# Optimization experiments

Measured on AMD Instinct MI355X. Metric: run time of the kernel, lower is better.

Reference implementation:

```python
import jax, jax.numpy as jnp
import numpy as np

B, S, E, H = 1, 4096, 768, 12
D = E // H  # headSize = 64

def setup_inputs() -> dict:
    key = jax.random.key(0)
    ks = jax.random.split(key, 7)
    scale = 1.0 / np.sqrt(E)
    return {
        "inputQueries": jax.random.normal(ks[0], (B, S, E), dtype=jnp.float32),
        "inputKeys":    jax.random.normal(ks[1], (B, S, E), dtype=jnp.float32),
        "inputValues":  jax.random.normal(ks[2], (B, S, E), dtype=jnp.float32),
        "Wq": jax.random.normal(ks[3], (E, E), dtype=jnp.float32) * scale,
        "Wk": jax.random.normal(ks[4], (E, E), dtype=jnp.float32) * scale,
        "Wv": jax.random.normal(ks[5], (E, E), dtype=jnp.float32) * scale,
        "Wo": jax.random.normal(ks[6], (E, E), dtype=jnp.float32) * scale,
    }

def reference(inputQueries, inputKeys, inputValues, Wq, Wk, Wv, Wo):
    # nn.Linear(x) = x @ W.T; weights stored as [out, in]
    q = inputQueries @ Wq.T  # [B,S,E]
    k = inputKeys @ Wk.T
    v = inputValues @ Wv.T
    # split heads -> [B,H,S,D]
    q = q.reshape(B, S, H, D).transpose(0, 2, 1, 3)
    k = k.reshape(B, S, H, D).transpose(0, 2, 1, 3)
    v = v.reshape(B, S, H, D).transpose(0, 2, 1, 3)
    # full QK^T scores [B,H,S,S] (faithful to the naive implementation)
    scores = jnp.einsum("bhqd,bhkd->bhqk", q, k) / jnp.sqrt(jnp.float32(D))
    attn = jax.nn.softmax(scores, axis=-1)
    # (mask path in original is a discarded non-inplace masked_fill -> no-op;
    #  dropout=0.0 -> identity)
    ctx = jnp.einsum("bhqk,bhkd->bhqd", attn, v)  # [B,H,S,D]
    ctx = ctx.transpose(0, 2, 1, 3).reshape(B, S, E)
    return ctx @ Wo.T
```

## Files before the change

kernel.cpp:

```cpp
#include <hip/hip_runtime.h>

#define SS 4096
#define EE 768
#define HH 12
#define DD 64

typedef __attribute__((ext_vector_type(4))) float f32x4;
typedef __attribute__((ext_vector_type(8))) _Float16 f16x8;
typedef __attribute__((ext_vector_type(4))) _Float16 f16x4;
typedef __attribute__((ext_vector_type(8))) unsigned short u16x8;

__global__ __launch_bounds__(256) void cast_kernel(
    const float* __restrict__ xq, const float* __restrict__ xk,
    const float* __restrict__ xv, const float* __restrict__ wq,
    const float* __restrict__ wk, const float* __restrict__ wv,
    const float* __restrict__ wo, _Float16* __restrict__ oxq,
    _Float16* __restrict__ oxk, _Float16* __restrict__ oxv,
    _Float16* __restrict__ owq, _Float16* __restrict__ owk,
    _Float16* __restrict__ owv, _Float16* __restrict__ owo) {
    const int seg = blockIdx.y;
    const float* src;
    _Float16* dst;
    int n;
    float s = 1.0f;
    switch (seg) {
        case 0: src = xq; dst = oxq; n = SS * EE; break;
        case 1: src = xk; dst = oxk; n = SS * EE; break;
        case 2: src = xv; dst = oxv; n = SS * EE; break;
        case 3: src = wq; dst = owq; n = EE * EE; s = 0.125f; break;
        case 4: src = wk; dst = owk; n = EE * EE; break;
        case 5: src = wv; dst = owv; n = EE * EE; break;
        default: src = wo; dst = owo; n = EE * EE; break;
    }
    const int i = (blockIdx.x * 256 + threadIdx.x) * 4;
    if (i < n) {
        const float4 v = *(const float4*)(src + i);
        f16x4 o;
        o[0] = (_Float16)(v.x * s); o[1] = (_Float16)(v.y * s);
        o[2] = (_Float16)(v.z * s); o[3] = (_Float16)(v.w * s);
        *(f16x4*)(dst + i) = o;
    }
}

template <bool F32OUT>
__device__ __forceinline__ void gemm_f16_body(const _Float16* __restrict__ A,
                                              const _Float16* __restrict__ B,
                                              void* __restrict__ Yv) {
    __shared__ _Float16 As[128 * 32];
    __shared__ _Float16 Bs[128 * 32];

    const int tid = threadIdx.x;
    const int w = tid >> 6, lane = tid & 63;
    const int g = lane >> 4, c = lane & 15;
    const int wr = (w >> 1) * 64, wc = (w & 1) * 64;
    const int m0 = blockIdx.y * 128, n0 = blockIdx.x * 128;

    f32x4 acc[4][4] = {};

    for (int k0 = 0; k0 < EE; k0 += 32) {
        __syncthreads();
#pragma unroll
        for (int i = 0; i < 2; ++i) {
            const int ca = tid + i * 256;
            __builtin_amdgcn_global_load_lds(
                (const __attribute__((address_space(1))) void*)(
                    A + (size_t)(m0 + (ca >> 2)) * EE + k0 + (ca & 3) * 8),
                (__attribute__((address_space(3))) void*)(As + ca * 8), 16, 0, 0);
            __builtin_amdgcn_global_load_lds(
                (const __attribute__((address_space(1))) void*)(
                    B + (size_t)(n0 + (ca >> 2)) * EE + k0 + (ca & 3) * 8),
                (__attribute__((address_space(3))) void*)(Bs + ca * 8), 16, 0, 0);
        }
        __syncthreads();

        f16x8 af[4], bf[4];
#pragma unroll
        for (int t = 0; t < 4; ++t) {
            af[t] = *(const f16x8*)(As + (wr + t * 16 + c) * 32 + g * 8);
            bf[t] = *(const f16x8*)(Bs + (wc + t * 16 + c) * 32 + g * 8);
        }
#pragma unroll
        for (int mt = 0; mt < 4; ++mt)
#pragma unroll
            for (int nt = 0; nt < 4; ++nt)
                acc[mt][nt] = __builtin_amdgcn_mfma_f32_16x16x32_f16(
                    af[mt], bf[nt], acc[mt][nt], 0, 0, 0);
    }

    if (F32OUT) {
        float* Y = (float*)Yv;
#pragma unroll
        for (int mt = 0; mt < 4; ++mt)
#pragma unroll
            for (int nt = 0; nt < 4; ++nt)
#pragma unroll
                for (int r = 0; r < 4; ++r)
                    Y[(size_t)(m0 + wr + mt * 16 + g * 4 + r) * EE +
                      n0 + wc + nt * 16 + c] = acc[mt][nt][r];
    } else {
        _Float16* Y = (_Float16*)Yv;
#pragma unroll
        for (int mt = 0; mt < 4; ++mt)
#pragma unroll
            for (int nt = 0; nt < 4; ++nt)
#pragma unroll
                for (int r = 0; r < 4; ++r)
                    Y[(size_t)(m0 + wr + mt * 16 + g * 4 + r) * EE +
                      n0 + wc + nt * 16 + c] = (_Float16)acc[mt][nt][r];
    }
}

__global__ __launch_bounds__(256) void qkv_gemm_kernel(
    const _Float16* __restrict__ Xq, const _Float16* __restrict__ Xk,
    const _Float16* __restrict__ Xv, const _Float16* __restrict__ Wq,
    const _Float16* __restrict__ Wk, const _Float16* __restrict__ Wv,
    _Float16* __restrict__ Yq, _Float16* __restrict__ Yk,
    _Float16* __restrict__ Yv) {
    const int z = blockIdx.z;
    const _Float16* X = (z == 0) ? Xq : (z == 1) ? Xk : Xv;
    const _Float16* W = (z == 0) ? Wq : (z == 1) ? Wk : Wv;
    _Float16* Y = (z == 0) ? Yq : (z == 1) ? Yk : Yv;
    gemm_f16_body<false>(X, W, (void*)Y);
}

__global__ __launch_bounds__(256) void out_gemm_kernel(
    const _Float16* __restrict__ X, const _Float16* __restrict__ W,
    float* __restrict__ Y) {
    gemm_f16_body<true>(X, W, (void*)Y);
}

__global__ __launch_bounds__(128) void attn_mfma_kernel(
    const _Float16* __restrict__ Qf, const _Float16* __restrict__ Kf,
    const _Float16* __restrict__ Vf, _Float16* __restrict__ C) {
    __shared__ _Float16 Ks[2][64 * 64];
    __shared__ unsigned char VtB[2][64 * 144];

    const int tid = threadIdx.x;
    const int bid = blockIdx.x;
    const int sw = (bid & 7) * 96 + (bid >> 3);
    const int h = sw >> 6;
    const int q0 = (sw & 63) * 64;
    const int w = tid >> 6;
    const int lane = tid & 63;
    const int g = lane >> 4;
    const int c = lane & 15;

    const int vr2 = tid >> 3;
    const int vm = tid & 7;

    f16x8 qa[2][2];
#pragma unroll
    for (int qf = 0; qf < 2; ++qf) {
        const _Float16* qp =
            Qf + (size_t)(q0 + w * 32 + qf * 16 + c) * EE + h * DD + g * 8;
        qa[qf][0] = *(const f16x8*)(qp);
        qa[qf][1] = *(const f16x8*)(qp + 32);
    }

    f32x4 o[2][4] = {};
    float m_q[2] = {-1e30f, -1e30f}, l_q[2] = {0.0f, 0.0f};
    u16x8 vreg[2][2];

#define ISSUE_K(buf, t0k)                                                     \
    {                                                                          \
        _Pragma("unroll") for (int i = 0; i < 4; ++i) {                        \
            const int L = i * 128 + tid;                                       \
            const int r_ = L >> 3;                                             \
            const int cc_ = (L & 7) ^ (r_ & 7);                                \
            __builtin_amdgcn_global_load_lds(                                  \
                (const __attribute__((address_space(1))) void*)(               \
                    Kf + (size_t)((t0k) + r_) * EE + h * DD + cc_ * 8),        \
                (__attribute__((address_space(3))) void*)(&Ks[buf][L * 8]),    \
                16, 0, 0);                                                     \
        }                                                                      \
    }
#define LOAD_V(t0v)                                                           \
    {                                                                          \
        _Pragma("unroll") for (int u = 0; u < 2; ++u) {                        \
            const int vrr = vr2 + 16 * u;                                      \
            const unsigned short* vp = (const unsigned short*)(                \
                Vf + (size_t)((t0v) + 2 * vrr) * EE + h * DD + vm * 8);        \
            vreg[u][0] = *(const u16x8*)(vp);                                  \
            vreg[u][1] = *(const u16x8*)(vp + EE);                             \
        }                                                                      \
    }
#define WRITE_V(buf)                                                          \
    {                                                                          \
        _Pragma("unroll") for (int u = 0; u < 2; ++u) {                        \
            const int vrr = vr2 + 16 * u;                                      \
            const int pu = 16 * (vrr >> 4) + 4 * ((vrr >> 1) & 3) +            \
                           2 * ((vrr >> 3) & 1) + (vrr & 1);                   \
            _Pragma("unroll") for (int j = 0; j < 8; ++j) {                    \
                const int d_ = vm * 8 + j;                                     \
                const unsigned off =                                           \
                    (unsigned)(144 * d_ + 4 * pu) ^ (unsigned)(vm << 4);       \
                *(unsigned int*)(&VtB[buf][off]) =                             \
                    (unsigned)vreg[u][0][j] | ((unsigned)vreg[u][1][j] << 16); \
            }                                                                  \
        }                                                                      \
    }

    ISSUE_K(0, 0);
    LOAD_V(0);
    WRITE_V(0);
    __syncthreads();

    for (int t = 0; t < SS / 64; ++t) {
        const int cur = t & 1;
        if (t < SS / 64 - 1) {
            ISSUE_K(cur ^ 1, (t + 1) * 64);
            LOAD_V((t + 1) * 64);
        }

        f32x4 sc[2][4] = {};
        __builtin_amdgcn_s_setprio(1);
#pragma unroll
        for (int ks = 0; ks < 2; ++ks) {
#pragma unroll
            for (int nt = 0; nt < 4; ++nt) {
                const f16x8 kbv = *(const f16x8*)(
                    &Ks[cur][(16 * nt + c) * 64 + (((g + 4 * ks) ^ (c & 7)) * 8)]);
#pragma unroll
                for (int qf = 0; qf < 2; ++qf)
                    sc[qf][nt] = __builtin_amdgcn_mfma_f32_16x16x32_f16(
                        kbv, qa[qf][ks], sc[qf][nt], 0, 0, 0);
            }
        }
        __builtin_amdgcn_s_setprio(0);

        f16x8 pb[2][2];
#pragma unroll
        for (int qf = 0; qf < 2; ++qf) {
            float mx0 = fmaxf(fmaxf(sc[qf][0][0], sc[qf][0][1]),
                              fmaxf(sc[qf][0][2], sc[qf][0][3]));
            float mx1 = fmaxf(fmaxf(sc[qf][1][0], sc[qf][1][1]),
                              fmaxf(sc[qf][1][2], sc[qf][1][3]));
            float mx2 = fmaxf(fmaxf(sc[qf][2][0], sc[qf][2][1]),
                              fmaxf(sc[qf][2][2], sc[qf][2][3]));
            float mx3 = fmaxf(fmaxf(sc[qf][3][0], sc[qf][3][1]),
                              fmaxf(sc[qf][3][2], sc[qf][3][3]));
            float mx = fmaxf(fmaxf(mx0, mx1), fmaxf(mx2, mx3));
            mx = fmaxf(mx, __shfl_xor(mx, 16));
            mx = fmaxf(mx, __shfl_xor(mx, 32));
            const float mnew = fmaxf(m_q[qf], mx);
            const float corr = __expf(m_q[qf] - mnew);
            m_q[qf] = mnew;
            float p[4][4];
            float rs = 0.0f;
#pragma unroll
            for (int nt = 0; nt < 4; ++nt)
#pragma unroll
                for (int r = 0; r < 4; ++r) {
                    p[nt][r] = __expf(sc[qf][nt][r] - mnew);
                    rs += p[nt][r];
                }
            rs += __shfl_xor(rs, 16);
            rs += __shfl_xor(rs, 32);
            l_q[qf] = l_q[qf] * corr + rs;
#pragma unroll
            for (int ks = 0; ks < 2; ++ks) {
                f16x8 t8;
                t8[0] = (_Float16)p[2 * ks][0];
                t8[1] = (_Float16)p[2 * ks][1];
                t8[2] = (_Float16)p[2 * ks][2];
                t8[3] = (_Float16)p[2 * ks][3];
                t8[4] = (_Float16)p[2 * ks + 1][0];
                t8[5] = (_Float16)p[2 * ks + 1][1];
                t8[6] = (_Float16)p[2 * ks + 1][2];
                t8[7] = (_Float16)p[2 * ks + 1][3];
                pb[qf][ks] = t8;
            }
#pragma unroll
            for (int dt = 0; dt < 4; ++dt)
                o[qf][dt] *= corr;
        }

        __builtin_amdgcn_s_setprio(1);
#pragma unroll
        for (int ks = 0; ks < 2; ++ks) {
#pragma unroll
            for (int dt = 0; dt < 4; ++dt) {
                const int d = 16 * dt + c;
                const unsigned off = (unsigned)(144 * d + 64 * ks + 16 * g) ^
                                     ((unsigned)((d >> 3) & 7) << 4);
                const f16x8 va = *(const f16x8*)(&VtB[cur][off]);
#pragma unroll
                for (int qf = 0; qf < 2; ++qf)
                    o[qf][dt] = __builtin_amdgcn_mfma_f32_16x16x32_f16(
                        va, pb[qf][ks], o[qf][dt], 0, 0, 0);
            }
        }
        __builtin_amdgcn_s_setprio(0);

        if (t < SS / 64 - 1) WRITE_V(cur ^ 1);
        __syncthreads();
    }

#pragma unroll
    for (int qf = 0; qf < 2; ++qf) {
        const float inv = 1.0f / l_q[qf];
        _Float16* cp = C + (size_t)(q0 + w * 32 + qf * 16 + c) * EE + h * DD;
#pragma unroll
        for (int dt = 0; dt < 4; ++dt) {
            f16x4 ov;
            ov[0] = (_Float16)(o[qf][dt][0] * inv);
            ov[1] = (_Float16)(o[qf][dt][1] * inv);
            ov[2] = (_Float16)(o[qf][dt][2] * inv);
            ov[3] = (_Float16)(o[qf][dt][3] * inv);
            *(f16x4*)(cp + 16 * dt + 4 * g) = ov;
        }
    }
#undef ISSUE_K
#undef LOAD_V
#undef WRITE_V
}

extern "C" void kernel_launch(void* const* d_in, const int* in_sizes, int n_in,
                              void* d_out, int out_size, void* d_ws, size_t ws_size,
                              hipStream_t stream) {
    const float* inQ = (const float*)d_in[0];
    const float* inK = (const float*)d_in[1];
    const float* inV = (const float*)d_in[2];
    const float* Wq = (const float*)d_in[3];
    const float* Wk = (const float*)d_in[4];
    const float* Wv = (const float*)d_in[5];
    const float* Wo = (const float*)d_in[6];
    float* out = (float*)d_out;

    const size_t SE = (size_t)SS * EE, E2 = (size_t)EE * EE;
    _Float16* p = (_Float16*)d_ws;
    _Float16* X16q = p; p += SE;
    _Float16* X16k = p; p += SE;
    _Float16* X16v = p; p += SE;
    _Float16* W16q = p; p += E2;
    _Float16* W16k = p; p += E2;
    _Float16* W16v = p; p += E2;
    _Float16* W16o = p; p += E2;
    _Float16* Qf = p; p += SE;
    _Float16* Kf = p; p += SE;
    _Float16* Vf = p; p += SE;
    _Float16* ctx = p; p += SE;

    cast_kernel<<<dim3(SS * EE / 1024, 7), dim3(256), 0, stream>>>(
        inQ, inK, inV, Wq, Wk, Wv, Wo,
        X16q, X16k, X16v, W16q, W16k, W16v, W16o);

    qkv_gemm_kernel<<<dim3(EE / 128, SS / 128, 3), dim3(256), 0, stream>>>(
        X16q, X16k, X16v, W16q, W16k, W16v, Qf, Kf, Vf);

    attn_mfma_kernel<<<dim3((SS / 64) * HH), dim3(128), 0, stream>>>(Qf, Kf, Vf, ctx);

    out_gemm_kernel<<<dim3(EE / 128, SS / 128), dim3(256), 0, stream>>>(ctx, W16o, out);
}
```

Before: 281.8 us.

## Use four waves of 16 query rows each and skip small online-softmax rescales

The attention kernel now launches 256 threads per block, and each wave handles 16 query rows instead of 32. Per-thread register use drops and more waves share each K/V tile loaded into LDS, which should improve occupancy and latency hiding. The running max and output rescale are now skipped when no lane's new max exceeds the old one by more than 8. Skipping keeps a stale max, which bounds exp values at e^8 and relies on fp16 P values staying in range. The trade-off is less register-level reuse of each K/V fragment read from LDS, since each wave now feeds only one query fragment per load.

```diff
diff --git a/kernel.cpp b/kernel.cpp
--- a/kernel.cpp
+++ b/kernel.cpp
@@ -129,7 +129,7 @@
     gemm_f16_body<true>(X, W, (void*)Y);
 }
 
-__global__ __launch_bounds__(128) void attn_mfma_kernel(
+__global__ __launch_bounds__(256) void attn_mfma_kernel(
     const _Float16* __restrict__ Qf, const _Float16* __restrict__ Kf,
     const _Float16* __restrict__ Vf, _Float16* __restrict__ C) {
     __shared__ _Float16 Ks[2][64 * 64];
@@ -145,26 +145,25 @@
     const int g = lane >> 4;
     const int c = lane & 15;
 
-    const int vr2 = tid >> 3;
+    const int vrr = tid >> 3;
     const int vm = tid & 7;
 
-    f16x8 qa[2][2];
-#pragma unroll
-    for (int qf = 0; qf < 2; ++qf) {
+    f16x8 qa[2];
+    {
         const _Float16* qp =
-            Qf + (size_t)(q0 + w * 32 + qf * 16 + c) * EE + h * DD + g * 8;
-        qa[qf][0] = *(const f16x8*)(qp);
-        qa[qf][1] = *(const f16x8*)(qp + 32);
-    }
-
-    f32x4 o[2][4] = {};
-    float m_q[2] = {-1e30f, -1e30f}, l_q[2] = {0.0f, 0.0f};
-    u16x8 vreg[2][2];
+            Qf + (size_t)(q0 + w * 16 + c) * EE + h * DD + g * 8;
+        qa[0] = *(const f16x8*)(qp);
+        qa[1] = *(const f16x8*)(qp + 32);
+    }
+
+    f32x4 o[4] = {};
+    float m_q = -1e30f, l_q = 0.0f;
+    u16x8 vreg[2];
 
 #define ISSUE_K(buf, t0k)                                                     \
     {                                                                          \
-        _Pragma("unroll") for (int i = 0; i < 4; ++i) {                        \
-            const int L = i * 128 + tid;                                       \
+        _Pragma("unroll") for (int i = 0; i < 2; ++i) {                        \
+            const int L = i * 256 + tid;                                       \
             const int r_ = L >> 3;                                             \
             const int cc_ = (L & 7) ^ (r_ & 7);                                \
             __builtin_amdgcn_global_load_lds(                                  \
@@ -176,27 +175,21 @@
     }
 #define LOAD_V(t0v)                                                           \
     {                                                                          \
-        _Pragma("unroll") for (int u = 0; u < 2; ++u) {                        \
-            const int vrr = vr2 + 16 * u;                                      \
-            const unsigned short* vp = (const unsigned short*)(                \
-                Vf + (size_t)((t0v) + 2 * vrr) * EE + h * DD + vm * 8);        \
-            vreg[u][0] = *(const u16x8*)(vp);                                  \
-            vreg[u][1] = *(const u16x8*)(vp + EE);                             \
-        }                                                                      \
+        const unsigned short* vp = (const unsigned short*)(                    \
+            Vf + (size_t)((t0v) + 2 * vrr) * EE + h * DD + vm * 8);            \
+        vreg[0] = *(const u16x8*)(vp);                                         \
+        vreg[1] = *(const u16x8*)(vp + EE);                                    \
     }
 #define WRITE_V(buf)                                                          \
     {                                                                          \
-        _Pragma("unroll") for (int u = 0; u < 2; ++u) {                        \
-            const int vrr = vr2 + 16 * u;                                      \
-            const int pu = 16 * (vrr >> 4) + 4 * ((vrr >> 1) & 3) +            \
-                           2 * ((vrr >> 3) & 1) + (vrr & 1);                   \
-            _Pragma("unroll") for (int j = 0; j < 8; ++j) {                    \
-                const int d_ = vm * 8 + j;                                     \
-                const unsigned off =                                           \
-                    (unsigned)(144 * d_ + 4 * pu) ^ (unsigned)(vm << 4);       \
-                *(unsigned int*)(&VtB[buf][off]) =                             \
-                    (unsigned)vreg[u][0][j] | ((unsigned)vreg[u][1][j] << 16); \
-            }                                                                  \
+        const int pu = 16 * (vrr >> 4) + 4 * ((vrr >> 1) & 3) +                \
+                       2 * ((vrr >> 3) & 1) + (vrr & 1);                       \
+        _Pragma("unroll") for (int j = 0; j < 8; ++j) {                        \
+            const int d_ = vm * 8 + j;                                         \
+            const unsigned off =                                               \
+                (unsigned)(144 * d_ + 4 * pu) ^ (unsigned)(vm << 4);           \
+            *(unsigned int*)(&VtB[buf][off]) =                                 \
+                (unsigned)vreg[0][j] | ((unsigned)vreg[1][j] << 16);           \
         }                                                                      \
     }
 
@@ -212,7 +205,7 @@
             LOAD_V((t + 1) * 64);
         }
 
-        f32x4 sc[2][4] = {};
+        f32x4 sc[4] = {};
         __builtin_amdgcn_s_setprio(1);
 #pragma unroll
         for (int ks = 0; ks < 2; ++ks) {
@@ -220,43 +213,42 @@
             for (int nt = 0; nt < 4; ++nt) {
                 const f16x8 kbv = *(const f16x8*)(
                     &Ks[cur][(16 * nt + c) * 64 + (((g + 4 * ks) ^ (c & 7)) * 8)]);
-#pragma unroll
-                for (int qf = 0; qf < 2; ++qf)
-                    sc[qf][nt] = __builtin_amdgcn_mfma_f32_16x16x32_f16(
-                        kbv, qa[qf][ks], sc[qf][nt], 0, 0, 0);
+                sc[nt] = __builtin_amdgcn_mfma_f32_16x16x32_f16(
+                    kbv, qa[ks], sc[nt], 0, 0, 0);
             }
         }
         __builtin_amdgcn_s_setprio(0);
 
-        f16x8 pb[2][2];
-#pragma unroll
-        for (int qf = 0; qf < 2; ++qf) {
-            float mx0 = fmaxf(fmaxf(sc[qf][0][0], sc[qf][0][1]),
-                              fmaxf(sc[qf][0][2], sc[qf][0][3]));
-            float mx1 = fmaxf(fmaxf(sc[qf][1][0], sc[qf][1][1]),
-                              fmaxf(sc[qf][1][2], sc[qf][1][3]));
-            float mx2 = fmaxf(fmaxf(sc[qf][2][0], sc[qf][2][1]),
-                              fmaxf(sc[qf][2][2], sc[qf][2][3]));
-            float mx3 = fmaxf(fmaxf(sc[qf][3][0], sc[qf][3][1]),
-                              fmaxf(sc[qf][3][2], sc[qf][3][3]));
+        f16x8 pb[2];
+        {
+            float mx0 = fmaxf(fmaxf(sc[0][0], sc[0][1]), fmaxf(sc[0][2], sc[0][3]));
+            float mx1 = fmaxf(fmaxf(sc[1][0], sc[1][1]), fmaxf(sc[1][2], sc[1][3]));
+            float mx2 = fmaxf(fmaxf(sc[2][0], sc[2][1]), fmaxf(sc[2][2], sc[2][3]));
+            float mx3 = fmaxf(fmaxf(sc[3][0], sc[3][1]), fmaxf(sc[3][2], sc[3][3]));
             float mx = fmaxf(fmaxf(mx0, mx1), fmaxf(mx2, mx3));
             mx = fmaxf(mx, __shfl_xor(mx, 16));
             mx = fmaxf(mx, __shfl_xor(mx, 32));
-            const float mnew = fmaxf(m_q[qf], mx);
-            const float corr = __expf(m_q[qf] - mnew);
-            m_q[qf] = mnew;
+            if (!__all(mx - m_q <= 8.0f)) {
+                const float mnew = fmaxf(m_q, mx);
+                const float corr = __expf(m_q - mnew);
+                m_q = mnew;
+                l_q *= corr;
+#pragma unroll
+                for (int dt = 0; dt < 4; ++dt)
+                    o[dt] *= corr;
+            }
             float p[4][4];
             float rs = 0.0f;
 #pragma unroll
             for (int nt = 0; nt < 4; ++nt)
 #pragma unroll
                 for (int r = 0; r < 4; ++r) {
-                    p[nt][r] = __expf(sc[qf][nt][r] - mnew);
+                    p[nt][r] = __expf(sc[nt][r] - m_q);
                     rs += p[nt][r];
                 }
             rs += __shfl_xor(rs, 16);
             rs += __shfl_xor(rs, 32);
-            l_q[qf] = l_q[qf] * corr + rs;
+            l_q += rs;
 #pragma unroll
             for (int ks = 0; ks < 2; ++ks) {
                 f16x8 t8;
@@ -268,11 +260,8 @@
                 t8[5] = (_Float16)p[2 * ks + 1][1];
                 t8[6] = (_Float16)p[2 * ks + 1][2];
                 t8[7] = (_Float16)p[2 * ks + 1][3];
-                pb[qf][ks] = t8;
+                pb[ks] = t8;
             }
-#pragma unroll
-            for (int dt = 0; dt < 4; ++dt)
-                o[qf][dt] *= corr;
         }
 
         __builtin_amdgcn_s_setprio(1);
@@ -284,10 +273,8 @@
                 const unsigned off = (unsigned)(144 * d + 64 * ks + 16 * g) ^
                                      ((unsigned)((d >> 3) & 7) << 4);
                 const f16x8 va = *(const f16x8*)(&VtB[cur][off]);
-#pragma unroll
-                for (int qf = 0; qf < 2; ++qf)
-                    o[qf][dt] = __builtin_amdgcn_mfma_f32_16x16x32_f16(
-                        va, pb[qf][ks], o[qf][dt], 0, 0, 0);
+                o[dt] = __builtin_amdgcn_mfma_f32_16x16x32_f16(
+                    va, pb[ks], o[dt], 0, 0, 0);
             }
         }
         __builtin_amdgcn_s_setprio(0);
@@ -296,17 +283,16 @@
         __syncthreads();
     }
 
-#pragma unroll
-    for (int qf = 0; qf < 2; ++qf) {
-        const float inv = 1.0f / l_q[qf];
-        _Float16* cp = C + (size_t)(q0 + w * 32 + qf * 16 + c) * EE + h * DD;
+    {
+        const float inv = 1.0f / l_q;
+        _Float16* cp = C + (size_t)(q0 + w * 16 + c) * EE + h * DD;
 #pragma unroll
         for (int dt = 0; dt < 4; ++dt) {
             f16x4 ov;
-            ov[0] = (_Float16)(o[qf][dt][0] * inv);
-            ov[1] = (_Float16)(o[qf][dt][1] * inv);
-            ov[2] = (_Float16)(o[qf][dt][2] * inv);
-            ov[3] = (_Float16)(o[qf][dt][3] * inv);
+            ov[0] = (_Float16)(o[dt][0] * inv);
+            ov[1] = (_Float16)(o[dt][1] * inv);
+            ov[2] = (_Float16)(o[dt][2] * inv);
+            ov[3] = (_Float16)(o[dt][3] * inv);
             *(f16x4*)(cp + 16 * dt + 4 * g) = ov;
         }
     }
@@ -348,7 +334,7 @@
     qkv_gemm_kernel<<<dim3(EE / 128, SS / 128, 3), dim3(256), 0, stream>>>(
         X16q, X16k, X16v, W16q, W16k, W16v, Qf, Kf, Vf);
 
-    attn_mfma_kernel<<<dim3((SS / 64) * HH), dim3(128), 0, stream>>>(Qf, Kf, Vf, ctx);
+    attn_mfma_kernel<<<dim3((SS / 64) * HH), dim3(256), 0, stream>>>(Qf, Kf, Vf, ctx);
 
     out_gemm_kernel<<<dim3(EE / 128, SS / 128), dim3(256), 0, stream>>>(ctx, W16o, out);
 }
```

Measured after the change: 253.9 us. 9.9% less time.
